# Optimization experiments

Measured on AMD Instinct MI355X. Metric: run time of the kernel, lower is better.

Reference implementation:

```python
import jax, jax.numpy as jnp
import numpy as np

TAG = 64
START = 0
END = 1
NEG = -10000.0


def setup_inputs() -> dict:
    key = jax.random.key(0)
    kf, kw, kl = jax.random.split(key, 3)
    B, T, K = 1024, 512, TAG
    feats = jax.random.normal(kf, (B, T, K), dtype=jnp.float32)
    w = jax.random.uniform(kw, (K, K), minval=-1.0 / K, maxval=1.0 / K, dtype=jnp.float32)
    # default adjacency: forbid transitions into start (row START) and out of end (col END)
    adj = jnp.zeros((K, K), jnp.float32).at[START, :].set(1.0).at[:, END].set(1.0)
    weights = w + NEG * adj
    lens = jax.random.randint(kl, (B,), 1, T + 1)  # 1..T inclusive
    return {"feats": feats, "weights": weights, "lens": lens}


def reference(feats, weights, lens):
    # feats: [B, T, K], weights: [K, K] with weights[next, prev], lens: [B]
    B, T, K = feats.shape
    init = jnp.full((B, K), NEG, feats.dtype).at[:, START].set(0.0)
    mask_tb = (jnp.arange(T)[None, :] < lens[:, None]).T  # [T, B]
    ident = jnp.arange(K, dtype=jnp.int32)

    def step(fv, inp):
        feat, m = inp  # feat: [B, K], m: [B]
        scores = fv[:, None, :] + weights[None, :, :]  # [B, next, prev]
        new_fv = jnp.max(scores, axis=-1) + feat       # emission added after max
        bptr = jnp.argmax(scores, axis=-1).astype(jnp.int32)
        fv2 = jnp.where(m[:, None], new_fv, fv)
        bptr2 = jnp.where(m[:, None], bptr, ident[None, :])  # identity keeps backtrace valid past len
        return fv2, bptr2

    fv, bptrs = jax.lax.scan(step, init, (jnp.swapaxes(feats, 0, 1), mask_tb))
    terminal = fv + weights[END][None, :]              # transition to end tag
    best_last = jnp.argmax(terminal, axis=-1)
    path_score = jnp.take_along_axis(terminal, best_last[:, None], axis=1)[:, 0]

    def back(tag, bp):  # tag: [B], bp: [B, K]
        prev = jnp.take_along_axis(bp, tag[:, None], axis=1)[:, 0]
        return prev, tag  # emit tag chosen at this timestep

    _, path = jax.lax.scan(back, best_last.astype(jnp.int32), bptrs, reverse=True)
    best_paths = jnp.swapaxes(path, 0, 1)  # [B, T]; positions >= lens[b] are padding
    return path_score, best_paths
```

## Files before the change

kernel.cpp:

```cpp
#include <hip/hip_runtime.h>

#define TAGS 64
#define MAXT 512
#define NEG  -10000.0f
#define CH   8

__global__ __launch_bounds__(64, 1) void crf_viterbi(
    const float* __restrict__ feats,
    const float* __restrict__ weights,
    const int*   __restrict__ lens,
    float*       __restrict__ out,
    int B, int T)
{
    const int b    = blockIdx.x;
    const int lane = threadIdx.x;
    const int len  = lens[b];

    __shared__ float fv[TAGS];
    __shared__ float fbuf[2][CH * TAGS];
    __shared__ unsigned char  bptr[MAXT * TAGS];
    __shared__ unsigned short path[MAXT];

    float4 w4[16];
    #pragma unroll
    for (int i = 0; i < 16; ++i)
        w4[i] = *reinterpret_cast<const float4*>(weights + lane * TAGS + i * 4);
    const float wEnd = weights[1 * TAGS + lane];

    fv[lane] = (lane == 0) ? 0.0f : NEG;

    const float* fb  = feats + (size_t)b * T * TAGS;
    const int    lim = len * TAGS - 4;

    float nf = NEG;

#define F3(a, b, c) fmaxf(fmaxf((a), (b)), (c))
#define M3(a, b, c) min(min((a), (b)), (c))

    auto step = [&](int cbuf, int i, int t) {
        const float feat = fbuf[cbuf][i * TAGS + lane];
        float4 fq[16];
        #pragma unroll
        for (int g = 0; g < 16; ++g)
            fq[g] = *reinterpret_cast<const float4*>(&fv[g * 4]);
        float4 c4[16];
        #pragma unroll
        for (int g = 0; g < 16; ++g) {
            c4[g].x = fq[g].x + w4[g].x;
            c4[g].y = fq[g].y + w4[g].y;
            c4[g].z = fq[g].z + w4[g].z;
            c4[g].w = fq[g].w + w4[g].w;
        }
        const float* c = reinterpret_cast<const float*>(c4);

        float v1[22];
        #pragma unroll
        for (int k = 0; k < 21; ++k) v1[k] = F3(c[3*k], c[3*k+1], c[3*k+2]);
        v1[21] = c[63];
        float v2[8];
        #pragma unroll
        for (int k = 0; k < 7; ++k) v2[k] = F3(v1[3*k], v1[3*k+1], v1[3*k+2]);
        v2[7] = v1[21];
        const float v30 = F3(v2[0], v2[1], v2[2]);
        const float v31 = F3(v2[3], v2[4], v2[5]);
        const float v32 = fmaxf(v2[6], v2[7]);
        const float m   = F3(v30, v31, v32);

        nf = m + feat;
        fv[lane] = nf;

        unsigned e[64];
        #pragma unroll
        for (int p = 0; p < 64; ++p) e[p] = (c[p] == m) ? (unsigned)p : 64u;
        unsigned u1[22];
        #pragma unroll
        for (int k = 0; k < 21; ++k) u1[k] = M3(e[3*k], e[3*k+1], e[3*k+2]);
        u1[21] = e[63];
        unsigned u2[8];
        #pragma unroll
        for (int k = 0; k < 7; ++k) u2[k] = M3(u1[3*k], u1[3*k+1], u1[3*k+2]);
        u2[7] = u1[21];
        const unsigned u30 = M3(u2[0], u2[1], u2[2]);
        const unsigned u31 = M3(u2[3], u2[4], u2[5]);
        const unsigned u32 = min(u2[6], u2[7]);
        const unsigned idx = M3(u30, u31, u32);

        bptr[t * TAGS + lane] = (unsigned char)idx;
    };

    {
        int o0 = 4 * lane;        if (o0 > lim) o0 = lim;
        int o1 = 256 + 4 * lane;  if (o1 > lim) o1 = lim;
        *reinterpret_cast<float4*>(&fbuf[0][4 * lane])       = *reinterpret_cast<const float4*>(fb + o0);
        *reinterpret_cast<float4*>(&fbuf[0][256 + 4 * lane]) = *reinterpret_cast<const float4*>(fb + o1);
    }
    float4 n0, n1;
    {
        int o0 = CH * TAGS + 4 * lane;        if (o0 > lim) o0 = lim;
        int o1 = CH * TAGS + 256 + 4 * lane;  if (o1 > lim) o1 = lim;
        n0 = *reinterpret_cast<const float4*>(fb + o0);
        n1 = *reinterpret_cast<const float4*>(fb + o1);
    }

    int cb = 0;
    const int nfull = len / CH;
    for (int c = 0; c < nfull; ++c) {
        #pragma unroll
        for (int i = 0; i < CH; ++i) step(cb, i, c * CH + i);
        *reinterpret_cast<float4*>(&fbuf[cb ^ 1][4 * lane])       = n0;
        *reinterpret_cast<float4*>(&fbuf[cb ^ 1][256 + 4 * lane]) = n1;
        {
            int o0 = (c + 2) * CH * TAGS + 4 * lane;        if (o0 > lim) o0 = lim;
            int o1 = (c + 2) * CH * TAGS + 256 + 4 * lane;  if (o1 > lim) o1 = lim;
            n0 = *reinterpret_cast<const float4*>(fb + o0);
            n1 = *reinterpret_cast<const float4*>(fb + o1);
        }
        cb ^= 1;
    }
    const int rem = len - nfull * CH;
    for (int i = 0; i < rem; ++i) step(cb, i, nfull * CH + i);

    float tv = nf + wEnd;
    int   ti = lane;
    #pragma unroll
    for (int off = 32; off >= 1; off >>= 1) {
        const float ov = __shfl_xor(tv, off);
        const int   oi = __shfl_xor(ti, off);
        if (ov > tv || (ov == tv && oi < ti)) { tv = ov; ti = oi; }
    }
    if (lane == 0) out[b] = tv;
    const int bestlast = ti;

    for (int t = lane; t < T; t += 64)
        if (t >= len - 1) path[t] = (unsigned short)bestlast;
    __builtin_amdgcn_wave_barrier();

    if (lane == 0) {
        int tag = bestlast;
        for (int t = len - 1; t >= 1; --t) {
            tag = bptr[t * TAGS + tag];
            path[t - 1] = (unsigned short)tag;
        }
    }
    __builtin_amdgcn_wave_barrier();

    float* pout = out + B + (size_t)b * T;
    for (int t = lane; t < T; t += 64)
        pout[t] = (float)path[t];
}

extern "C" void kernel_launch(void* const* d_in, const int* in_sizes, int n_in,
                              void* d_out, int out_size, void* d_ws, size_t ws_size,
                              hipStream_t stream) {
    const float* feats   = (const float*)d_in[0];
    const float* weights = (const float*)d_in[1];
    const int*   lens    = (const int*)d_in[2];
    float*       out     = (float*)d_out;

    const int B = in_sizes[2];
    const int T = in_sizes[0] / (B * TAGS);

    crf_viterbi<<<dim3(B), dim3(64), 0, stream>>>(feats, weights, lens, out, B, T);
}
```

Before: 425.5 us.

## Sort sequences by length and pair long with short per block

Adds a single-block bitonic sort of the lengths to build a permutation, then launches half as many blocks, each running two sequences in turn: the i-th longest paired with the i-th shortest. This evens out the serial work per block so the tail of long sequences no longer sets the kernel time. It also requests 18 KB of dynamic shared memory as a throttle, which caps how many blocks share a CU. The cost is an extra kernel launch with a tiny sort and fewer blocks to hide latency. The paired path only runs when B is 1024 and the workspace is large enough.

```diff
diff --git a/kernel.cpp b/kernel.cpp
--- a/kernel.cpp
+++ b/kernel.cpp
@@ -5,16 +5,43 @@
 #define NEG  -10000.0f
 #define CH   8
 
+__global__ void sort_lens_kernel(const int* __restrict__ lens, int B,
+                                 int* __restrict__ perm) {
+    __shared__ unsigned s[1024];
+    const int tid = threadIdx.x;
+    for (int i = tid; i < 1024; i += 256) {
+        const unsigned l = (i < B) ? (unsigned)lens[i] : 0xFFFFu;
+        s[i] = (l << 16) | (unsigned)i;
+    }
+    __syncthreads();
+    for (int k = 2; k <= 1024; k <<= 1) {
+        for (int j = k >> 1; j > 0; j >>= 1) {
+            for (int i = tid; i < 1024; i += 256) {
+                const int ixj = i ^ j;
+                if (ixj > i) {
+                    const unsigned a = s[i], c = s[ixj];
+                    if ((a > c) == ((i & k) == 0)) { s[i] = c; s[ixj] = a; }
+                }
+            }
+            __syncthreads();
+        }
+    }
+    for (int i = tid; i < 1024; i += 256)
+        if (i < B) perm[i] = (int)(s[i] & 0xFFFFu);
+}
+
 __global__ __launch_bounds__(64, 1) void crf_viterbi(
     const float* __restrict__ feats,
     const float* __restrict__ weights,
     const int*   __restrict__ lens,
+    const int*   __restrict__ perm,
     float*       __restrict__ out,
-    int B, int T)
+    int B, int T, int npass)
 {
-    const int b    = blockIdx.x;
+    extern __shared__ char dyn_throttle[];
+    (void)dyn_throttle;
+
     const int lane = threadIdx.x;
-    const int len  = lens[b];
 
     __shared__ float fv[TAGS];
     __shared__ float fbuf[2][CH * TAGS];
@@ -27,126 +54,133 @@
         w4[i] = *reinterpret_cast<const float4*>(weights + lane * TAGS + i * 4);
     const float wEnd = weights[1 * TAGS + lane];
 
-    fv[lane] = (lane == 0) ? 0.0f : NEG;
-
-    const float* fb  = feats + (size_t)b * T * TAGS;
-    const int    lim = len * TAGS - 4;
-
-    float nf = NEG;
-
 #define F3(a, b, c) fmaxf(fmaxf((a), (b)), (c))
 #define M3(a, b, c) min(min((a), (b)), (c))
 
-    auto step = [&](int cbuf, int i, int t) {
-        const float feat = fbuf[cbuf][i * TAGS + lane];
-        float4 fq[16];
-        #pragma unroll
-        for (int g = 0; g < 16; ++g)
-            fq[g] = *reinterpret_cast<const float4*>(&fv[g * 4]);
-        float4 c4[16];
-        #pragma unroll
-        for (int g = 0; g < 16; ++g) {
-            c4[g].x = fq[g].x + w4[g].x;
-            c4[g].y = fq[g].y + w4[g].y;
-            c4[g].z = fq[g].z + w4[g].z;
-            c4[g].w = fq[g].w + w4[g].w;
-        }
-        const float* c = reinterpret_cast<const float*>(c4);
-
-        float v1[22];
-        #pragma unroll
-        for (int k = 0; k < 21; ++k) v1[k] = F3(c[3*k], c[3*k+1], c[3*k+2]);
-        v1[21] = c[63];
-        float v2[8];
-        #pragma unroll
-        for (int k = 0; k < 7; ++k) v2[k] = F3(v1[3*k], v1[3*k+1], v1[3*k+2]);
-        v2[7] = v1[21];
-        const float v30 = F3(v2[0], v2[1], v2[2]);
-        const float v31 = F3(v2[3], v2[4], v2[5]);
-        const float v32 = fmaxf(v2[6], v2[7]);
-        const float m   = F3(v30, v31, v32);
-
-        nf = m + feat;
-        fv[lane] = nf;
-
-        unsigned e[64];
-        #pragma unroll
-        for (int p = 0; p < 64; ++p) e[p] = (c[p] == m) ? (unsigned)p : 64u;
-        unsigned u1[22];
-        #pragma unroll
-        for (int k = 0; k < 21; ++k) u1[k] = M3(e[3*k], e[3*k+1], e[3*k+2]);
-        u1[21] = e[63];
-        unsigned u2[8];
-        #pragma unroll
-        for (int k = 0; k < 7; ++k) u2[k] = M3(u1[3*k], u1[3*k+1], u1[3*k+2]);
-        u2[7] = u1[21];
-        const unsigned u30 = M3(u2[0], u2[1], u2[2]);
-        const unsigned u31 = M3(u2[3], u2[4], u2[5]);
-        const unsigned u32 = min(u2[6], u2[7]);
-        const unsigned idx = M3(u30, u31, u32);
-
-        bptr[t * TAGS + lane] = (unsigned char)idx;
-    };
-
-    {
-        int o0 = 4 * lane;        if (o0 > lim) o0 = lim;
-        int o1 = 256 + 4 * lane;  if (o1 > lim) o1 = lim;
-        *reinterpret_cast<float4*>(&fbuf[0][4 * lane])       = *reinterpret_cast<const float4*>(fb + o0);
-        *reinterpret_cast<float4*>(&fbuf[0][256 + 4 * lane]) = *reinterpret_cast<const float4*>(fb + o1);
-    }
-    float4 n0, n1;
-    {
-        int o0 = CH * TAGS + 4 * lane;        if (o0 > lim) o0 = lim;
-        int o1 = CH * TAGS + 256 + 4 * lane;  if (o1 > lim) o1 = lim;
-        n0 = *reinterpret_cast<const float4*>(fb + o0);
-        n1 = *reinterpret_cast<const float4*>(fb + o1);
-    }
-
-    int cb = 0;
-    const int nfull = len / CH;
-    for (int c = 0; c < nfull; ++c) {
-        #pragma unroll
-        for (int i = 0; i < CH; ++i) step(cb, i, c * CH + i);
-        *reinterpret_cast<float4*>(&fbuf[cb ^ 1][4 * lane])       = n0;
-        *reinterpret_cast<float4*>(&fbuf[cb ^ 1][256 + 4 * lane]) = n1;
+    for (int pass = 0; pass < npass; ++pass) {
+        const int bb = (npass == 2)
+                         ? perm[pass == 0 ? (B - 1 - blockIdx.x) : blockIdx.x]
+                         : blockIdx.x;
+        const int len = lens[bb];
+
+        fv[lane] = (lane == 0) ? 0.0f : NEG;
+
+        const float* fb  = feats + (size_t)bb * T * TAGS;
+        const int    lim = len * TAGS - 4;
+
+        float nf = NEG;
+
+        auto step = [&](int cbuf, int i, int t) {
+            const float feat = fbuf[cbuf][i * TAGS + lane];
+            float4 fq[16];
+            #pragma unroll
+            for (int g = 0; g < 16; ++g)
+                fq[g] = *reinterpret_cast<const float4*>(&fv[g * 4]);
+            float4 c4[16];
+            #pragma unroll
+            for (int g = 0; g < 16; ++g) {
+                c4[g].x = fq[g].x + w4[g].x;
+                c4[g].y = fq[g].y + w4[g].y;
+                c4[g].z = fq[g].z + w4[g].z;
+                c4[g].w = fq[g].w + w4[g].w;
+            }
+            const float* c = reinterpret_cast<const float*>(c4);
+
+            float v1[22];
+            #pragma unroll
+            for (int k = 0; k < 21; ++k) v1[k] = F3(c[3*k], c[3*k+1], c[3*k+2]);
+            v1[21] = c[63];
+            float v2[8];
+            #pragma unroll
+            for (int k = 0; k < 7; ++k) v2[k] = F3(v1[3*k], v1[3*k+1], v1[3*k+2]);
+            v2[7] = v1[21];
+            const float v30 = F3(v2[0], v2[1], v2[2]);
+            const float v31 = F3(v2[3], v2[4], v2[5]);
+            const float v32 = fmaxf(v2[6], v2[7]);
+            const float m   = F3(v30, v31, v32);
+
+            nf = m + feat;
+            fv[lane] = nf;
+
+            unsigned e[64];
+            #pragma unroll
+            for (int p = 0; p < 64; ++p) e[p] = (c[p] == m) ? (unsigned)p : 64u;
+            unsigned u1[22];
+            #pragma unroll
+            for (int k = 0; k < 21; ++k) u1[k] = M3(e[3*k], e[3*k+1], e[3*k+2]);
+            u1[21] = e[63];
+            unsigned u2[8];
+            #pragma unroll
+            for (int k = 0; k < 7; ++k) u2[k] = M3(u1[3*k], u1[3*k+1], u1[3*k+2]);
+            u2[7] = u1[21];
+            const unsigned u30 = M3(u2[0], u2[1], u2[2]);
+            const unsigned u31 = M3(u2[3], u2[4], u2[5]);
+            const unsigned u32 = min(u2[6], u2[7]);
+            const unsigned idx = M3(u30, u31, u32);
+
+            bptr[t * TAGS + lane] = (unsigned char)idx;
+        };
+
         {
-            int o0 = (c + 2) * CH * TAGS + 4 * lane;        if (o0 > lim) o0 = lim;
-            int o1 = (c + 2) * CH * TAGS + 256 + 4 * lane;  if (o1 > lim) o1 = lim;
+            int o0 = 4 * lane;        if (o0 > lim) o0 = lim;
+            int o1 = 256 + 4 * lane;  if (o1 > lim) o1 = lim;
+            *reinterpret_cast<float4*>(&fbuf[0][4 * lane])       = *reinterpret_cast<const float4*>(fb + o0);
+            *reinterpret_cast<float4*>(&fbuf[0][256 + 4 * lane]) = *reinterpret_cast<const float4*>(fb + o1);
+        }
+        float4 n0, n1;
+        {
+            int o0 = CH * TAGS + 4 * lane;        if (o0 > lim) o0 = lim;
+            int o1 = CH * TAGS + 256 + 4 * lane;  if (o1 > lim) o1 = lim;
             n0 = *reinterpret_cast<const float4*>(fb + o0);
             n1 = *reinterpret_cast<const float4*>(fb + o1);
         }
-        cb ^= 1;
-    }
-    const int rem = len - nfull * CH;
-    for (int i = 0; i < rem; ++i) step(cb, i, nfull * CH + i);
-
-    float tv = nf + wEnd;
-    int   ti = lane;
-    #pragma unroll
-    for (int off = 32; off >= 1; off >>= 1) {
-        const float ov = __shfl_xor(tv, off);
-        const int   oi = __shfl_xor(ti, off);
-        if (ov > tv || (ov == tv && oi < ti)) { tv = ov; ti = oi; }
-    }
-    if (lane == 0) out[b] = tv;
-    const int bestlast = ti;
-
-    for (int t = lane; t < T; t += 64)
-        if (t >= len - 1) path[t] = (unsigned short)bestlast;
-    __builtin_amdgcn_wave_barrier();
-
-    if (lane == 0) {
-        int tag = bestlast;
-        for (int t = len - 1; t >= 1; --t) {
-            tag = bptr[t * TAGS + tag];
-            path[t - 1] = (unsigned short)tag;
-        }
-    }
-    __builtin_amdgcn_wave_barrier();
-
-    float* pout = out + B + (size_t)b * T;
-    for (int t = lane; t < T; t += 64)
-        pout[t] = (float)path[t];
+
+        int cb = 0;
+        const int nfull = len / CH;
+        for (int c = 0; c < nfull; ++c) {
+            #pragma unroll
+            for (int i = 0; i < CH; ++i) step(cb, i, c * CH + i);
+            *reinterpret_cast<float4*>(&fbuf[cb ^ 1][4 * lane])       = n0;
+            *reinterpret_cast<float4*>(&fbuf[cb ^ 1][256 + 4 * lane]) = n1;
+            {
+                int o0 = (c + 2) * CH * TAGS + 4 * lane;        if (o0 > lim) o0 = lim;
+                int o1 = (c + 2) * CH * TAGS + 256 + 4 * lane;  if (o1 > lim) o1 = lim;
+                n0 = *reinterpret_cast<const float4*>(fb + o0);
+                n1 = *reinterpret_cast<const float4*>(fb + o1);
+            }
+            cb ^= 1;
+        }
+        const int rem = len - nfull * CH;
+        for (int i = 0; i < rem; ++i) step(cb, i, nfull * CH + i);
+
+        float tv = nf + wEnd;
+        int   ti = lane;
+        #pragma unroll
+        for (int off = 32; off >= 1; off >>= 1) {
+            const float ov = __shfl_xor(tv, off);
+            const int   oi = __shfl_xor(ti, off);
+            if (ov > tv || (ov == tv && oi < ti)) { tv = ov; ti = oi; }
+        }
+        if (lane == 0) out[bb] = tv;
+        const int bestlast = ti;
+
+        for (int t = lane; t < T; t += 64)
+            if (t >= len - 1) path[t] = (unsigned short)bestlast;
+        __builtin_amdgcn_wave_barrier();
+
+        if (lane == 0) {
+            int tag = bestlast;
+            for (int t = len - 1; t >= 1; --t) {
+                tag = bptr[t * TAGS + tag];
+                path[t - 1] = (unsigned short)tag;
+            }
+        }
+        __builtin_amdgcn_wave_barrier();
+
+        float* pout = out + B + (size_t)bb * T;
+        for (int t = lane; t < T; t += 64)
+            pout[t] = (float)path[t];
+    }
 }
 
 extern "C" void kernel_launch(void* const* d_in, const int* in_sizes, int n_in,
@@ -156,9 +190,18 @@
     const float* weights = (const float*)d_in[1];
     const int*   lens    = (const int*)d_in[2];
     float*       out     = (float*)d_out;
+    int*         perm    = (int*)d_ws;
 
     const int B = in_sizes[2];
     const int T = in_sizes[0] / (B * TAGS);
 
-    crf_viterbi<<<dim3(B), dim3(64), 0, stream>>>(feats, weights, lens, out, B, T);
+    const bool paired = (B == 1024) && (ws_size >= 1024 * sizeof(int));
+    if (paired) {
+        sort_lens_kernel<<<dim3(1), dim3(256), 0, stream>>>(lens, B, perm);
+        crf_viterbi<<<dim3(B / 2), dim3(64), 18432, stream>>>(
+            feats, weights, lens, perm, out, B, T, 2);
+    } else {
+        crf_viterbi<<<dim3(B), dim3(64), 18432, stream>>>(
+            feats, weights, lens, perm, out, B, T, 1);
+    }
 }
```

Result: slower. 465.9 us (+9.5%).
